# Optimization experiments

Measured on AMD Instinct MI355X. Metric: run time of the kernel, lower is better.

Reference implementation:

```python
import jax, jax.numpy as jnp
import numpy as np

N_NODES = 100000
N_EDGES = 1600000
IN_DIM = 256
OUT_DIM = 64
NEG_SLOPE = 0.01  # torch F.leaky_relu default


def setup_inputs() -> dict:
    key = jax.random.key(0)
    k1, k2, k3, k4 = jax.random.split(key, 4)
    h = jax.random.normal(k1, (N_NODES, IN_DIM), dtype=jnp.float32)
    # xavier_normal with gain for relu ~ sqrt(2)*sqrt(2/(fan_in+fan_out))
    W_fc = jax.random.normal(k2, (OUT_DIM, IN_DIM), dtype=jnp.float32) * (np.sqrt(2.0) * np.sqrt(2.0 / (IN_DIM + OUT_DIM)))
    a_attn = jax.random.normal(k3, (1, 2 * OUT_DIM), dtype=jnp.float32) * (np.sqrt(2.0) * np.sqrt(2.0 / (2 * OUT_DIM + 1)))
    edge_index = jax.random.randint(k4, (2, N_EDGES), 0, N_NODES, dtype=jnp.int64)
    return {"h": h, "W_fc": W_fc, "a_attn": a_attn, "edge_index": edge_index}


def reference(h, W_fc, a_attn, edge_index):
    src, dst = edge_index[0], edge_index[1]
    n = h.shape[0]
    z = h @ W_fc.T  # [N, out_dim]
    # attn_fc(cat([z_src, z_dst])) == z_src @ a_l + z_dst @ a_r
    a_l = a_attn[0, :OUT_DIM]
    a_r = a_attn[0, OUT_DIM:]
    s_src = z @ a_l  # [N]
    s_dst = z @ a_r  # [N]
    e = jax.nn.leaky_relu(s_src[src] + s_dst[dst], NEG_SLOPE)  # [E]
    # segment softmax over incoming edges of each dst node (numerically stable)
    emax = jax.ops.segment_max(e, dst, num_segments=n)
    emax = jnp.where(jnp.isfinite(emax), emax, 0.0)  # empty segments
    ex = jnp.exp(e - emax[dst])
    denom = jax.ops.segment_sum(ex, dst, num_segments=n)
    alpha = ex / jnp.where(denom > 0, denom, 1.0)[dst]  # [E]
    # weighted scatter-sum aggregation
    h_out = jax.ops.segment_sum(alpha[:, None] * z[src], dst, num_segments=n)  # [N, out_dim]
    return h_out
```

## Files before the change

### kernel.cpp

```cpp
#include <hip/hip_runtime.h>

#define N_NODES 100000
#define N_EDGES 1600000
#define IN_DIM  256
#define OUT_DIM 64
#define NEG_SLOPE 0.01f

#define BSHIFT 8
#define NBUCK  ((N_NODES + 255) / 256)
#define BCAP   5120
#define EPT    16
#define PART_NB ((N_EDGES + 4095) / 4096)

typedef __attribute__((ext_vector_type(8))) short bf16x8;
typedef __attribute__((ext_vector_type(4))) float f32x4;

__device__ __forceinline__ short f2bf(float f) {
    unsigned u = __float_as_uint(f);
    return (short)((u + 0x7fffu + ((u >> 16) & 1u)) >> 16);
}
__device__ __forceinline__ float bflo(unsigned p) { return __uint_as_float(p << 16); }
__device__ __forceinline__ float bfhi(unsigned p) { return __uint_as_float(p & 0xffff0000u); }

__global__ __launch_bounds__(256) void k_wcvt(const float* __restrict__ W,
                                              ushort* __restrict__ wb) {
    int i = (blockIdx.x * 256 + threadIdx.x) * 4;
    if (i >= OUT_DIM * IN_DIM) return;
    float4 v = *(const float4*)(W + i);
    ushort4 o;
    o.x = (ushort)f2bf(v.x); o.y = (ushort)f2bf(v.y);
    o.z = (ushort)f2bf(v.z); o.w = (ushort)f2bf(v.w);
    *(ushort4*)(wb + i) = o;
}

__global__ __launch_bounds__(256) void k1_gemm(
        const float* __restrict__ h, const ushort* __restrict__ wb,
        const float* __restrict__ a_attn, ushort* __restrict__ zb,
        float* __restrict__ s_src, float* __restrict__ s_dst) {
    const int lane = threadIdx.x & 63;
    const int w    = threadIdx.x >> 6;
    const int g    = lane >> 4;
    const int r16  = lane & 15;
    const int rb   = blockIdx.x * 64 + w * 16;

    f32x4 acc[4];
#pragma unroll
    for (int nr = 0; nr < 4; ++nr) acc[nr] = (f32x4){0.f, 0.f, 0.f, 0.f};

    int r = rb + r16;
    const float* hp = h + (size_t)(r < N_NODES ? r : N_NODES - 1) * IN_DIM;

#pragma unroll
    for (int ks = 0; ks < 8; ++ks) {
        const int k0 = ks * 32 + g * 8;
        float4 lo = *(const float4*)(hp + k0);
        float4 hi = *(const float4*)(hp + k0 + 4);
        bf16x8 a;
        a[0] = f2bf(lo.x); a[1] = f2bf(lo.y); a[2] = f2bf(lo.z); a[3] = f2bf(lo.w);
        a[4] = f2bf(hi.x); a[5] = f2bf(hi.y); a[6] = f2bf(hi.z); a[7] = f2bf(hi.w);
        bf16x8 b[4];
#pragma unroll
        for (int nr = 0; nr < 4; ++nr)
            b[nr] = *(const bf16x8*)(wb + (size_t)(nr * 16 + r16) * IN_DIM + k0);
#pragma unroll
        for (int nr = 0; nr < 4; ++nr)
            acc[nr] = __builtin_amdgcn_mfma_f32_16x16x32_bf16(a, b[nr], acc[nr], 0, 0, 0);
    }

    float al[4], ar[4];
#pragma unroll
    for (int nr = 0; nr < 4; ++nr) {
        al[nr] = a_attn[nr * 16 + r16];
        ar[nr] = a_attn[OUT_DIM + nr * 16 + r16];
    }
#pragma unroll
    for (int rr = 0; rr < 4; ++rr) {
        float ps = 0.f, pd = 0.f;
#pragma unroll
        for (int nr = 0; nr < 4; ++nr) {
            ps = fmaf(acc[nr][rr], al[nr], ps);
            pd = fmaf(acc[nr][rr], ar[nr], pd);
        }
#pragma unroll
        for (int m = 1; m < 16; m <<= 1) {
            ps += __shfl_xor(ps, m, 64);
            pd += __shfl_xor(pd, m, 64);
        }
        int row = rb + g * 4 + rr;
        if (r16 == 0 && row < N_NODES) { s_src[row] = ps; s_dst[row] = pd; }
    }
#pragma unroll
    for (int nr = 0; nr < 4; ++nr)
#pragma unroll
        for (int rr = 0; rr < 4; ++rr) {
            int row = rb + g * 4 + rr;
            if (row < N_NODES)
                zb[(size_t)row * OUT_DIM + nr * 16 + r16] = (ushort)f2bf(acc[nr][rr]);
        }
}

__global__ void k_initcur(int* __restrict__ gcur) {
    int i = blockIdx.x * 256 + threadIdx.x;
    if (i < NBUCK) gcur[i] = i * BCAP;
}

__global__ __launch_bounds__(256) void k_part(const int* __restrict__ src,
                                              const int* __restrict__ dst,
                                              int* __restrict__ gcur,
                                              int* __restrict__ packed) {
    __shared__ int hist[NBUCK];
    __shared__ int base[NBUCK];
    const int t = threadIdx.x;
    for (int i = t; i < NBUCK; i += 256) hist[i] = 0;
    __syncthreads();

    const size_t e0 = (size_t)blockIdx.x * 4096;
    int myd[EPT];
#pragma unroll
    for (int k = 0; k < EPT; ++k) {
        size_t e = e0 + t + (size_t)k * 256;
        int d = (e < N_EDGES) ? dst[e] : -1;
        myd[k] = d;
        if (d >= 0) atomicAdd(&hist[d >> BSHIFT], 1);
    }
    __syncthreads();
    for (int i = t; i < NBUCK; i += 256) {
        int c = hist[i];
        base[i] = (c > 0) ? atomicAdd(&gcur[i], c) : 0;
        hist[i] = 0;
    }
    __syncthreads();
#pragma unroll
    for (int k = 0; k < EPT; ++k) {
        int d = myd[k];
        if (d >= 0) {
            size_t e = e0 + t + (size_t)k * 256;
            int s = src[e];
            int b = d >> BSHIFT;
            int r = atomicAdd(&hist[b], 1);
            int pos = base[b] + r;
            if (pos < (b + 1) * BCAP)
                packed[pos] = s | ((d & 255) << 17);
        }
    }
}

__global__ __launch_bounds__(512) void k_bscan(const int* __restrict__ gcur,
                                               int* __restrict__ bbase,
                                               int* __restrict__ rowptr) {
    __shared__ int ws[8];
    int t = threadIdx.x;
    int v = (t < NBUCK) ? (gcur[t] - t * BCAP) : 0;
    if (v > BCAP) v = BCAP;
    int lane = t & 63, wv = t >> 6;
    int incl = v;
#pragma unroll
    for (int off = 1; off < 64; off <<= 1) {
        int n = __shfl_up(incl, off, 64);
        if (lane >= off) incl += n;
    }
    if (lane == 63) ws[wv] = incl;
    __syncthreads();
    int woff = 0;
    for (int w = 0; w < wv; ++w) woff += ws[w];
    if (t < NBUCK) bbase[t] = woff + incl - v;
    if (t == 0) rowptr[N_NODES] = N_EDGES;
}

__global__ __launch_bounds__(256) void k_csr(const int* __restrict__ gcur,
                                             const int* __restrict__ bbase,
                                             const int* __restrict__ packed,
                                             int* __restrict__ rowptr,
                                             int* __restrict__ col) {
    __shared__ int cnt[256];
    __shared__ int lptr[256];
    __shared__ int wtot[4];
    const int b = blockIdx.x, t = threadIdx.x;
    int m = gcur[b] - b * BCAP; if (m > BCAP) m = BCAP;
    int nb = N_NODES - (b << BSHIFT); if (nb > 256) nb = 256;
    const int gbase = bbase[b];
    const size_t reg = (size_t)b * BCAP;

    cnt[t] = 0;
    __syncthreads();
    for (int i = t; i < m; i += 256)
        atomicAdd(&cnt[packed[reg + i] >> 17], 1);
    __syncthreads();

    int v = cnt[t];
    int lane = t & 63, wv = t >> 6;
    int incl = v;
#pragma unroll
    for (int off = 1; off < 64; off <<= 1) {
        int n = __shfl_up(incl, off, 64);
        if (lane >= off) incl += n;
    }
    if (lane == 63) wtot[wv] = incl;
    __syncthreads();
    int woff = 0;
    for (int w = 0; w < wv; ++w) woff += wtot[w];
    lptr[t] = woff + incl - v;
    if (t < nb) rowptr[(b << BSHIFT) + t] = gbase + lptr[t];
    cnt[t] = 0;
    __syncthreads();

    for (int i = t; i < m; i += 256) {
        int p = packed[reg + i];
        int dl = p >> 17;
        int r = atomicAdd(&cnt[dl], 1);
        col[gbase + lptr[dl] + r] = p & 0x1FFFF;
    }
}

__global__ __launch_bounds__(256) void k_gather(
        const int* __restrict__ rowptr, const int* __restrict__ col,
        const float* __restrict__ s_src, const float* __restrict__ s_dst,
        const ushort* __restrict__ zb, float* __restrict__ out) {
    const int lane = threadIdx.x & 63;
    const int d = blockIdx.x * 4 + (threadIdx.x >> 6);
    const int jg = lane >> 3;
    const int q  = lane & 7;
    const int beg = rowptr[d], end = rowptr[d + 1];
    const int deg = end - beg;
    const float sdd = s_dst[d];

    float acc[8];
#pragma unroll
    for (int k = 0; k < 8; ++k) acc[k] = 0.f;
    float dsum = 0.f;

    for (int cbeg = beg; cbeg < end; cbeg += 64) {
        int cn = end - cbeg; if (cn > 64) cn = 64;
        int sl = 0; float exl = 0.f;
        if (lane < cn) {
            sl = col[cbeg + lane];
            float t = s_src[sl] + sdd;
            t = t > 0.f ? t : t * NEG_SLOPE;
            exl = __expf(t);
        }
        dsum += exl;
        for (int j0 = 0; j0 < cn; j0 += 8) {
            int e = j0 + jg;
            int ei = e & 63;
            int   s  = __shfl(sl,  ei, 64);
            float ex = __shfl(exl, ei, 64);
            if (e < cn) {
                uint4 v = *(const uint4*)(zb + (size_t)s * OUT_DIM + q * 8);
                acc[0] = fmaf(ex, bflo(v.x), acc[0]);
                acc[1] = fmaf(ex, bfhi(v.x), acc[1]);
                acc[2] = fmaf(ex, bflo(v.y), acc[2]);
                acc[3] = fmaf(ex, bfhi(v.y), acc[3]);
                acc[4] = fmaf(ex, bflo(v.z), acc[4]);
                acc[5] = fmaf(ex, bfhi(v.z), acc[5]);
                acc[6] = fmaf(ex, bflo(v.w), acc[6]);
                acc[7] = fmaf(ex, bfhi(v.w), acc[7]);
            }
        }
    }

#pragma unroll
    for (int off = 8; off < 64; off <<= 1)
#pragma unroll
        for (int k = 0; k < 8; ++k)
            acc[k] += __shfl_xor(acc[k], off, 64);
#pragma unroll
    for (int off = 1; off < 64; off <<= 1) dsum += __shfl_xor(dsum, off, 64);

    if (jg == 0) {
        float inv = (deg > 0) ? 1.f / dsum : 0.f;
        float4 o0, o1;
        o0.x = acc[0] * inv; o0.y = acc[1] * inv; o0.z = acc[2] * inv; o0.w = acc[3] * inv;
        o1.x = acc[4] * inv; o1.y = acc[5] * inv; o1.z = acc[6] * inv; o1.w = acc[7] * inv;
        *(float4*)(out + (size_t)d * OUT_DIM + q * 8)     = o0;
        *(float4*)(out + (size_t)d * OUT_DIM + q * 8 + 4) = o1;
    }
}

extern "C" void kernel_launch(void* const* d_in, const int* in_sizes, int n_in,
                              void* d_out, int out_size, void* d_ws, size_t ws_size,
                              hipStream_t stream) {
    const float* h      = (const float*)d_in[0];
    const float* W      = (const float*)d_in[1];
    const float* a_attn = (const float*)d_in[2];
    const int*   ei     = (const int*)d_in[3];
    const int* src = ei;
    const int* dst = ei + N_EDGES;
    float* out = (float*)d_out;

    auto rup = [](size_t x) { return (x + 511) & ~size_t(511); };
    char* ws = (char*)d_ws;
    ushort* zb    = (ushort*)ws; ws += rup((size_t)N_NODES * OUT_DIM * 2);
    ushort* wb    = (ushort*)ws; ws += rup((size_t)OUT_DIM * IN_DIM * 2);
    float* s_src  = (float*)ws;  ws += rup((size_t)N_NODES * 4);
    float* s_dst  = (float*)ws;  ws += rup((size_t)N_NODES * 4);
    int*   rowptr = (int*)ws;    ws += rup(((size_t)N_NODES + 1) * 4);
    int*   gcur   = (int*)ws;    ws += rup((size_t)NBUCK * 4);
    int*   bbase  = (int*)ws;    ws += rup((size_t)NBUCK * 4);
    int*   packed = (int*)ws;    ws += rup((size_t)NBUCK * BCAP * 4);
    int*   col    = (int*)ws;    ws += rup((size_t)N_EDGES * 4);

    k_initcur<<<(NBUCK + 255) / 256, 256, 0, stream>>>(gcur);
    k_wcvt  <<<(OUT_DIM * IN_DIM / 4 + 255) / 256, 256, 0, stream>>>(W, wb);
    k1_gemm <<<(N_NODES + 63) / 64, 256, 0, stream>>>(h, wb, a_attn, zb, s_src, s_dst);
    k_part  <<<PART_NB, 256, 0, stream>>>(src, dst, gcur, packed);
    k_bscan <<<1, 512, 0, stream>>>(gcur, bbase, rowptr);
    k_csr   <<<NBUCK, 256, 0, stream>>>(gcur, bbase, packed, rowptr, col);
    k_gather<<<N_NODES / 4, 256, 0, stream>>>(rowptr, col, s_src, s_dst, zb, out);
}
```

Baseline: 283.3 us.

## Fuse GEMM and edge partition into one launch, fold scans into CSR build

Merges the projection GEMM and the dst-bucket partition into one kernel with block ranges split by blockIdx, so the compute-bound GEMM and the atomic-heavy partition run at the same time. The gcur init moves into the weight-convert kernel as a zero count, and the separate bucket scan kernel is dropped: each CSR block works out its own global base by summing the clamped counts of earlier buckets. Launch count falls from seven to four, at the cost of every CSR block redundantly reading and reducing up to 391 bucket counts.

```diff
diff --git a/kernel.cpp b/kernel.cpp
--- a/kernel.cpp
+++ b/kernel.cpp
@@ -11,6 +11,7 @@
 #define BCAP   5120
 #define EPT    16
 #define PART_NB ((N_EDGES + 4095) / 4096)
+#define GEMM_NB ((N_NODES + 63) / 64)
 
 typedef __attribute__((ext_vector_type(8))) short bf16x8;
 typedef __attribute__((ext_vector_type(4))) float f32x4;
@@ -23,8 +24,11 @@
 __device__ __forceinline__ float bfhi(unsigned p) { return __uint_as_float(p & 0xffff0000u); }
 
 __global__ __launch_bounds__(256) void k_wcvt(const float* __restrict__ W,
-                                              ushort* __restrict__ wb) {
-    int i = (blockIdx.x * 256 + threadIdx.x) * 4;
+                                              ushort* __restrict__ wb,
+                                              int* __restrict__ gcur) {
+    int gid = blockIdx.x * 256 + threadIdx.x;
+    if (gid < NBUCK) gcur[gid] = 0;
+    int i = gid * 4;
     if (i >= OUT_DIM * IN_DIM) return;
     float4 v = *(const float4*)(W + i);
     ushort4 o;
@@ -33,163 +37,144 @@
     *(ushort4*)(wb + i) = o;
 }
 
-__global__ __launch_bounds__(256) void k1_gemm(
+__global__ __launch_bounds__(256) void k_fused(
         const float* __restrict__ h, const ushort* __restrict__ wb,
         const float* __restrict__ a_attn, ushort* __restrict__ zb,
-        float* __restrict__ s_src, float* __restrict__ s_dst) {
-    const int lane = threadIdx.x & 63;
-    const int w    = threadIdx.x >> 6;
-    const int g    = lane >> 4;
-    const int r16  = lane & 15;
-    const int rb   = blockIdx.x * 64 + w * 16;
-
-    f32x4 acc[4];
-#pragma unroll
-    for (int nr = 0; nr < 4; ++nr) acc[nr] = (f32x4){0.f, 0.f, 0.f, 0.f};
-
-    int r = rb + r16;
-    const float* hp = h + (size_t)(r < N_NODES ? r : N_NODES - 1) * IN_DIM;
-
-#pragma unroll
-    for (int ks = 0; ks < 8; ++ks) {
-        const int k0 = ks * 32 + g * 8;
-        float4 lo = *(const float4*)(hp + k0);
-        float4 hi = *(const float4*)(hp + k0 + 4);
-        bf16x8 a;
-        a[0] = f2bf(lo.x); a[1] = f2bf(lo.y); a[2] = f2bf(lo.z); a[3] = f2bf(lo.w);
-        a[4] = f2bf(hi.x); a[5] = f2bf(hi.y); a[6] = f2bf(hi.z); a[7] = f2bf(hi.w);
-        bf16x8 b[4];
+        float* __restrict__ s_src, float* __restrict__ s_dst,
+        const int* __restrict__ src, const int* __restrict__ dst,
+        int* __restrict__ gcur, int* __restrict__ packed) {
+    if (blockIdx.x < GEMM_NB) {
+        const int lane = threadIdx.x & 63;
+        const int w    = threadIdx.x >> 6;
+        const int g    = lane >> 4;
+        const int r16  = lane & 15;
+        const int rb   = blockIdx.x * 64 + w * 16;
+
+        f32x4 acc[4];
+#pragma unroll
+        for (int nr = 0; nr < 4; ++nr) acc[nr] = (f32x4){0.f, 0.f, 0.f, 0.f};
+
+        int r = rb + r16;
+        const float* hp = h + (size_t)(r < N_NODES ? r : N_NODES - 1) * IN_DIM;
+
+#pragma unroll
+        for (int ks = 0; ks < 8; ++ks) {
+            const int k0 = ks * 32 + g * 8;
+            float4 lo = *(const float4*)(hp + k0);
+            float4 hi = *(const float4*)(hp + k0 + 4);
+            bf16x8 a;
+            a[0] = f2bf(lo.x); a[1] = f2bf(lo.y); a[2] = f2bf(lo.z); a[3] = f2bf(lo.w);
+            a[4] = f2bf(hi.x); a[5] = f2bf(hi.y); a[6] = f2bf(hi.z); a[7] = f2bf(hi.w);
+            bf16x8 b[4];
+#pragma unroll
+            for (int nr = 0; nr < 4; ++nr)
+                b[nr] = *(const bf16x8*)(wb + (size_t)(nr * 16 + r16) * IN_DIM + k0);
+#pragma unroll
+            for (int nr = 0; nr < 4; ++nr)
+                acc[nr] = __builtin_amdgcn_mfma_f32_16x16x32_bf16(a, b[nr], acc[nr], 0, 0, 0);
+        }
+
+        float al[4], ar[4];
+#pragma unroll
+        for (int nr = 0; nr < 4; ++nr) {
+            al[nr] = a_attn[nr * 16 + r16];
+            ar[nr] = a_attn[OUT_DIM + nr * 16 + r16];
+        }
+#pragma unroll
+        for (int rr = 0; rr < 4; ++rr) {
+            float ps = 0.f, pd = 0.f;
+#pragma unroll
+            for (int nr = 0; nr < 4; ++nr) {
+                ps = fmaf(acc[nr][rr], al[nr], ps);
+                pd = fmaf(acc[nr][rr], ar[nr], pd);
+            }
+#pragma unroll
+            for (int m = 1; m < 16; m <<= 1) {
+                ps += __shfl_xor(ps, m, 64);
+                pd += __shfl_xor(pd, m, 64);
+            }
+            int row = rb + g * 4 + rr;
+            if (r16 == 0 && row < N_NODES) { s_src[row] = ps; s_dst[row] = pd; }
+        }
 #pragma unroll
         for (int nr = 0; nr < 4; ++nr)
-            b[nr] = *(const bf16x8*)(wb + (size_t)(nr * 16 + r16) * IN_DIM + k0);
-#pragma unroll
-        for (int nr = 0; nr < 4; ++nr)
-            acc[nr] = __builtin_amdgcn_mfma_f32_16x16x32_bf16(a, b[nr], acc[nr], 0, 0, 0);
-    }
-
-    float al[4], ar[4];
-#pragma unroll
-    for (int nr = 0; nr < 4; ++nr) {
-        al[nr] = a_attn[nr * 16 + r16];
-        ar[nr] = a_attn[OUT_DIM + nr * 16 + r16];
-    }
-#pragma unroll
-    for (int rr = 0; rr < 4; ++rr) {
-        float ps = 0.f, pd = 0.f;
-#pragma unroll
-        for (int nr = 0; nr < 4; ++nr) {
-            ps = fmaf(acc[nr][rr], al[nr], ps);
-            pd = fmaf(acc[nr][rr], ar[nr], pd);
-        }
-#pragma unroll
-        for (int m = 1; m < 16; m <<= 1) {
-            ps += __shfl_xor(ps, m, 64);
-            pd += __shfl_xor(pd, m, 64);
-        }
-        int row = rb + g * 4 + rr;
-        if (r16 == 0 && row < N_NODES) { s_src[row] = ps; s_dst[row] = pd; }
-    }
-#pragma unroll
-    for (int nr = 0; nr < 4; ++nr)
-#pragma unroll
-        for (int rr = 0; rr < 4; ++rr) {
-            int row = rb + g * 4 + rr;
-            if (row < N_NODES)
-                zb[(size_t)row * OUT_DIM + nr * 16 + r16] = (ushort)f2bf(acc[nr][rr]);
-        }
-}
-
-__global__ void k_initcur(int* __restrict__ gcur) {
-    int i = blockIdx.x * 256 + threadIdx.x;
-    if (i < NBUCK) gcur[i] = i * BCAP;
-}
-
-__global__ __launch_bounds__(256) void k_part(const int* __restrict__ src,
-                                              const int* __restrict__ dst,
-                                              int* __restrict__ gcur,
-                                              int* __restrict__ packed) {
-    __shared__ int hist[NBUCK];
-    __shared__ int base[NBUCK];
-    const int t = threadIdx.x;
-    for (int i = t; i < NBUCK; i += 256) hist[i] = 0;
-    __syncthreads();
-
-    const size_t e0 = (size_t)blockIdx.x * 4096;
-    int myd[EPT];
-#pragma unroll
-    for (int k = 0; k < EPT; ++k) {
-        size_t e = e0 + t + (size_t)k * 256;
-        int d = (e < N_EDGES) ? dst[e] : -1;
-        myd[k] = d;
-        if (d >= 0) atomicAdd(&hist[d >> BSHIFT], 1);
-    }
-    __syncthreads();
-    for (int i = t; i < NBUCK; i += 256) {
-        int c = hist[i];
-        base[i] = (c > 0) ? atomicAdd(&gcur[i], c) : 0;
-        hist[i] = 0;
-    }
-    __syncthreads();
-#pragma unroll
-    for (int k = 0; k < EPT; ++k) {
-        int d = myd[k];
-        if (d >= 0) {
+#pragma unroll
+            for (int rr = 0; rr < 4; ++rr) {
+                int row = rb + g * 4 + rr;
+                if (row < N_NODES)
+                    zb[(size_t)row * OUT_DIM + nr * 16 + r16] = (ushort)f2bf(acc[nr][rr]);
+            }
+    } else {
+        __shared__ int hist[NBUCK];
+        __shared__ int base[NBUCK];
+        const int t = threadIdx.x;
+        for (int i = t; i < NBUCK; i += 256) hist[i] = 0;
+        __syncthreads();
+
+        const size_t e0 = (size_t)(blockIdx.x - GEMM_NB) * 4096;
+        int myd[EPT];
+#pragma unroll
+        for (int k = 0; k < EPT; ++k) {
             size_t e = e0 + t + (size_t)k * 256;
-            int s = src[e];
-            int b = d >> BSHIFT;
-            int r = atomicAdd(&hist[b], 1);
-            int pos = base[b] + r;
-            if (pos < (b + 1) * BCAP)
-                packed[pos] = s | ((d & 255) << 17);
-        }
-    }
-}
-
-__global__ __launch_bounds__(512) void k_bscan(const int* __restrict__ gcur,
-                                               int* __restrict__ bbase,
-                                               int* __restrict__ rowptr) {
-    __shared__ int ws[8];
-    int t = threadIdx.x;
-    int v = (t < NBUCK) ? (gcur[t] - t * BCAP) : 0;
-    if (v > BCAP) v = BCAP;
-    int lane = t & 63, wv = t >> 6;
-    int incl = v;
-#pragma unroll
-    for (int off = 1; off < 64; off <<= 1) {
-        int n = __shfl_up(incl, off, 64);
-        if (lane >= off) incl += n;
-    }
-    if (lane == 63) ws[wv] = incl;
-    __syncthreads();
-    int woff = 0;
-    for (int w = 0; w < wv; ++w) woff += ws[w];
-    if (t < NBUCK) bbase[t] = woff + incl - v;
-    if (t == 0) rowptr[N_NODES] = N_EDGES;
+            int d = (e < N_EDGES) ? dst[e] : -1;
+            myd[k] = d;
+            if (d >= 0) atomicAdd(&hist[d >> BSHIFT], 1);
+        }
+        __syncthreads();
+        for (int i = t; i < NBUCK; i += 256) {
+            int c = hist[i];
+            base[i] = (c > 0) ? atomicAdd(&gcur[i], c) : 0;
+            hist[i] = 0;
+        }
+        __syncthreads();
+#pragma unroll
+        for (int k = 0; k < EPT; ++k) {
+            int d = myd[k];
+            if (d >= 0) {
+                size_t e = e0 + t + (size_t)k * 256;
+                int s = src[e];
+                int b = d >> BSHIFT;
+                int r = atomicAdd(&hist[b], 1);
+                int off = base[b] + r;
+                if (off < BCAP)
+                    packed[(size_t)b * BCAP + off] = s | ((d & 255) << 17);
+            }
+        }
+    }
 }
 
 __global__ __launch_bounds__(256) void k_csr(const int* __restrict__ gcur,
-                                             const int* __restrict__ bbase,
                                              const int* __restrict__ packed,
                                              int* __restrict__ rowptr,
                                              int* __restrict__ col) {
     __shared__ int cnt[256];
     __shared__ int lptr[256];
     __shared__ int wtot[4];
+    __shared__ int wred[4];
     const int b = blockIdx.x, t = threadIdx.x;
-    int m = gcur[b] - b * BCAP; if (m > BCAP) m = BCAP;
+    const int lane = t & 63, wv = t >> 6;
+
+    int v = 0;
+    if (t < NBUCK && t < b)       { int c = gcur[t];       v += (c > BCAP ? BCAP : c); }
+    if (t + 256 < NBUCK && t + 256 < b) { int c = gcur[t + 256]; v += (c > BCAP ? BCAP : c); }
+#pragma unroll
+    for (int off = 1; off < 64; off <<= 1) v += __shfl_xor(v, off, 64);
+    if (lane == 0) wred[wv] = v;
+
+    int m = gcur[b]; if (m > BCAP) m = BCAP;
     int nb = N_NODES - (b << BSHIFT); if (nb > 256) nb = 256;
-    const int gbase = bbase[b];
     const size_t reg = (size_t)b * BCAP;
 
     cnt[t] = 0;
     __syncthreads();
+    const int gbase = wred[0] + wred[1] + wred[2] + wred[3];
+
     for (int i = t; i < m; i += 256)
         atomicAdd(&cnt[packed[reg + i] >> 17], 1);
     __syncthreads();
 
-    int v = cnt[t];
-    int lane = t & 63, wv = t >> 6;
-    int incl = v;
+    int c = cnt[t];
+    int incl = c;
 #pragma unroll
     for (int off = 1; off < 64; off <<= 1) {
         int n = __shfl_up(incl, off, 64);
@@ -199,8 +184,9 @@
     __syncthreads();
     int woff = 0;
     for (int w = 0; w < wv; ++w) woff += wtot[w];
-    lptr[t] = woff + incl - v;
+    lptr[t] = woff + incl - c;
     if (t < nb) rowptr[(b << BSHIFT) + t] = gbase + lptr[t];
+    if (b == 0 && t == 0) rowptr[N_NODES] = N_EDGES;
     cnt[t] = 0;
     __syncthreads();
 
@@ -295,15 +281,12 @@
     float* s_dst  = (float*)ws;  ws += rup((size_t)N_NODES * 4);
     int*   rowptr = (int*)ws;    ws += rup(((size_t)N_NODES + 1) * 4);
     int*   gcur   = (int*)ws;    ws += rup((size_t)NBUCK * 4);
-    int*   bbase  = (int*)ws;    ws += rup((size_t)NBUCK * 4);
     int*   packed = (int*)ws;    ws += rup((size_t)NBUCK * BCAP * 4);
     int*   col    = (int*)ws;    ws += rup((size_t)N_EDGES * 4);
 
-    k_initcur<<<(NBUCK + 255) / 256, 256, 0, stream>>>(gcur);
-    k_wcvt  <<<(OUT_DIM * IN_DIM / 4 + 255) / 256, 256, 0, stream>>>(W, wb);
-    k1_gemm <<<(N_NODES + 63) / 64, 256, 0, stream>>>(h, wb, a_attn, zb, s_src, s_dst);
-    k_part  <<<PART_NB, 256, 0, stream>>>(src, dst, gcur, packed);
-    k_bscan <<<1, 512, 0, stream>>>(gcur, bbase, rowptr);
-    k_csr   <<<NBUCK, 256, 0, stream>>>(gcur, bbase, packed, rowptr, col);
+    k_wcvt  <<<(OUT_DIM * IN_DIM / 4 + 255) / 256, 256, 0, stream>>>(W, wb, gcur);
+    k_fused <<<GEMM_NB + PART_NB, 256, 0, stream>>>(h, wb, a_attn, zb, s_src, s_dst,
+                                                    src, dst, gcur, packed);
+    k_csr   <<<NBUCK, 256, 0, stream>>>(gcur, packed, rowptr, col);
     k_gather<<<N_NODES / 4, 256, 0, stream>>>(rowptr, col, s_src, s_dst, zb, out);
 }
```

New measurement: 266.8 us. 1.06x faster.
